# Optimization experiments

Measured on AMD Instinct MI355X. Metric: run time of the kernel, lower is better.

The kernel has to match this reference:

```python
import jax, jax.numpy as jnp
import numpy as np

B, S, D, H = 4, 2048, 2048, 16
DH = D // H


def setup_inputs() -> dict:
    key = jax.random.key(0)
    ks = jax.random.split(key, 11)
    p = 0.02  # keep pre-softmax logits in a sane range
    return {
        "x": jax.random.normal(ks[0], (B, S, D), jnp.float32),
        "Wq": jax.random.normal(ks[1], (D, D), jnp.float32) * p,
        "bq": jax.random.normal(ks[2], (D,), jnp.float32) * p,
        "Wk": jax.random.normal(ks[3], (D, D), jnp.float32) * p,
        "bk": jax.random.normal(ks[4], (D,), jnp.float32) * p,
        "Wv": jax.random.normal(ks[5], (D, D), jnp.float32) * p,
        "bv": jax.random.normal(ks[6], (D,), jnp.float32) * p,
        "Wo": jax.random.normal(ks[7], (D, D), jnp.float32) * p,
        "bo": jax.random.normal(ks[8], (D,), jnp.float32) * p,
        "spiral_weight": jax.random.normal(ks[9], (H,), jnp.float32),
        "helix_rotation": jax.random.normal(ks[10], (D,), jnp.float32),
    }


def reference(x, Wq, bq, Wk, bk, Wv, bv, Wo, bo, spiral_weight, helix_rotation):
    b, s, d = x.shape
    h, dh = H, d // H
    # projections (torch Linear: x @ W.T + b), split into heads
    q = (x @ Wq.T + bq).reshape(b, s, h, dh)
    k = (x @ Wk.T + bk).reshape(b, s, h, dh)
    v = (x @ Wv.T + bv).reshape(b, s, h, dh)
    # cos/sin helix gating, applied per (head, head_dim) channel
    rot = helix_rotation.reshape(h, dh)
    q = q * jnp.cos(rot)
    k = k * jnp.sin(rot)
    # per-head scaled scores: [b,h,s,s]
    scores = jnp.einsum("bshd,bthd->bhst", q, k) / np.sqrt(dh).astype(np.float32)
    scores = scores * spiral_weight[None, :, None, None]
    attn = jax.nn.softmax(scores, axis=-1)
    out = jnp.einsum("bhst,bthd->bshd", attn, v).reshape(b, s, d)
    return out @ Wo.T + bo
```

## Files before the change

kernel.cpp:

```cpp
#include <hip/hip_runtime.h>
#include <math.h>

#define B_ 4
#define S_ 2048
#define D_ 2048
#define H_ 16
#define DH_ 128

typedef unsigned short u16;
typedef unsigned int u32;
typedef u16 u16x8 __attribute__((ext_vector_type(8)));
typedef __bf16 bf16x8 __attribute__((ext_vector_type(8)));
typedef float f32x4 __attribute__((ext_vector_type(4)));

__device__ inline u16 f2bf(float f) {
    unsigned int u = __builtin_bit_cast(unsigned int, f);
    unsigned int lsb = (u >> 16) & 1u;
    u += 0x7fffu + lsb;
    return (u16)(u >> 16);
}

__device__ inline f32x4 mfma16(u16x8 a, u16x8 b, f32x4 c) {
    return __builtin_amdgcn_mfma_f32_16x16x32_bf16(
        __builtin_bit_cast(bf16x8, a), __builtin_bit_cast(bf16x8, b), c, 0, 0, 0);
}

__device__ inline void gl2lds16(const u16* g, u16* l) {
    __builtin_amdgcn_global_load_lds(
        (const __attribute__((address_space(1))) void*)g,
        (__attribute__((address_space(3))) void*)l, 16, 0, 0);
}

__device__ inline void block_barrier() {
    asm volatile("" ::: "memory");
    __builtin_amdgcn_s_barrier();
    asm volatile("" ::: "memory");
}

__global__ __launch_bounds__(256) void cvt_f32_bf16(const float* __restrict__ src,
                                                    u16* __restrict__ dst, int n8) {
    int i = blockIdx.x * 256 + threadIdx.x;
    if (i >= n8) return;
    const float4* s = (const float4*)src + (size_t)i * 2;
    float4 a = s[0], b = s[1];
    u16x8 o;
    o[0] = f2bf(a.x); o[1] = f2bf(a.y); o[2] = f2bf(a.z); o[3] = f2bf(a.w);
    o[4] = f2bf(b.x); o[5] = f2bf(b.y); o[6] = f2bf(b.z); o[7] = f2bf(b.w);
    *((u16x8*)dst + i) = o;
}

template <int GATE, int VOUT, typename OutT>
__global__ __launch_bounds__(512, 2) void gemm256(const u16* __restrict__ A,
                                                  const u16* __restrict__ Bw,
                                                  const float* __restrict__ bias,
                                                  const float* __restrict__ helix,
                                                  OutT* __restrict__ C,
                                                  int M, int N, int K) {
    __shared__ __align__(16) u16 As[2][256 * 64];
    __shared__ __align__(16) u16 Bs[2][256 * 64];

    const int tid = threadIdx.x;
    const int lane = tid & 63, w = tid >> 6;
    const int lr = lane & 15, quad = lane >> 4;
    const int wm = w & 1, wn = w >> 1;
    const int tm = blockIdx.y, tn = blockIdx.x;
    const int NT = K >> 6;

    const u16* Asrc = A + (size_t)(tm * 256) * K;
    const u16* Bsrc = Bw + (size_t)(tn * 256) * K;

    u32 go[4][2];
    u32 lo[4][2];
#pragma unroll
    for (int q = 0; q < 2; ++q) {
        const int seg = w * 2 + q;
        const int i0 = seg * 8 + (lane >> 3);
        const int s0 = seg * 8;
        int row = (i0 & 63) | ((i0 >> 6) << 7);
        int rb = (s0 & 63) | ((s0 >> 6) << 7);
        go[0][q] = (u32)row * K + (((lane & 7) ^ (row & 7)) << 3);
        lo[0][q] = rb << 6;
        row += 64; rb += 64;
        go[3][q] = (u32)row * K + (((lane & 7) ^ (row & 7)) << 3);
        lo[3][q] = rb << 6;
        row = (i0 & 31) | ((i0 >> 5) << 6);
        rb = (s0 & 31) | ((s0 >> 5) << 6);
        go[1][q] = (u32)row * K + (((lane & 7) ^ (row & 7)) << 3);
        lo[1][q] = rb << 6;
        row += 32; rb += 32;
        go[2][q] = (u32)row * K + (((lane & 7) ^ (row & 7)) << 3);
        lo[2][q] = rb << 6;
    }

#define STAGE(u, tt)                                                          \
    do {                                                                      \
        const int kt_ = (((tt) < NT) ? (tt) : (NT - 1)) << 6;                 \
        const u16* gb_ = ((u) == 1 || (u) == 2) ? Bsrc : Asrc;                \
        u16* lb_ = ((u) == 1 || (u) == 2) ? Bs[(tt) & 1] : As[(tt) & 1];      \
        gl2lds16(gb_ + go[u][0] + kt_, lb_ + lo[u][0]);                       \
        gl2lds16(gb_ + go[u][1] + kt_, lb_ + lo[u][1]);                       \
    } while (0)

    const int koff0 = (quad * 8) ^ ((lr & 7) * 8);
    const int koff1 = (32 + quad * 8) ^ ((lr & 7) * 8);
    const int rA = wm * 128 + lr;
    const int rB = wn * 64 + lr;

    f32x4 zero = {0.f, 0.f, 0.f, 0.f};
    f32x4 acc[8][4];
#pragma unroll
    for (int im = 0; im < 8; ++im)
#pragma unroll
        for (int jn = 0; jn < 4; ++jn) acc[im][jn] = zero;

    u16x8 af[4][2], bf[4][2];

    STAGE(0, 0); STAGE(1, 0); STAGE(2, 0); STAGE(3, 0);
    STAGE(0, 1); STAGE(1, 1); STAGE(2, 1);
    asm volatile("s_waitcnt vmcnt(6)" ::: "memory");
    block_barrier();

    for (int t = 0; t < NT; ++t) {
        const u16* Ab = As[t & 1];
        const u16* Bb = Bs[t & 1];

#pragma unroll
        for (int im = 0; im < 4; ++im) {
            af[im][0] = *(const u16x8*)&Ab[(rA + im * 16) * 64 + koff0];
            af[im][1] = *(const u16x8*)&Ab[(rA + im * 16) * 64 + koff1];
        }
#pragma unroll
        for (int jn = 0; jn < 2; ++jn) {
            bf[jn][0] = *(const u16x8*)&Bb[(rB + jn * 16) * 64 + koff0];
            bf[jn][1] = *(const u16x8*)&Bb[(rB + jn * 16) * 64 + koff1];
        }
        STAGE(3, t + 1);
        block_barrier();
        asm volatile("s_waitcnt lgkmcnt(0)" ::: "memory");
        __builtin_amdgcn_s_setprio(1);
#pragma unroll
        for (int s = 0; s < 2; ++s)
#pragma unroll
            for (int im = 0; im < 4; ++im)
#pragma unroll
                for (int jn = 0; jn < 2; ++jn)
                    acc[im][jn] = mfma16(af[im][s], bf[jn][s], acc[im][jn]);
        __builtin_amdgcn_s_setprio(0);
        block_barrier();

#pragma unroll
        for (int jn = 2; jn < 4; ++jn) {
            bf[jn][0] = *(const u16x8*)&Bb[(rB + jn * 16) * 64 + koff0];
            bf[jn][1] = *(const u16x8*)&Bb[(rB + jn * 16) * 64 + koff1];
        }
        STAGE(0, t + 2);
        block_barrier();
        asm volatile("s_waitcnt lgkmcnt(0)" ::: "memory");
        __builtin_amdgcn_s_setprio(1);
#pragma unroll
        for (int s = 0; s < 2; ++s)
#pragma unroll
            for (int im = 0; im < 4; ++im)
#pragma unroll
                for (int jn = 2; jn < 4; ++jn)
                    acc[im][jn] = mfma16(af[im][s], bf[jn][s], acc[im][jn]);
        __builtin_amdgcn_s_setprio(0);
        block_barrier();

#pragma unroll
        for (int im = 0; im < 4; ++im) {
            af[im][0] = *(const u16x8*)&Ab[(rA + 64 + im * 16) * 64 + koff0];
            af[im][1] = *(const u16x8*)&Ab[(rA + 64 + im * 16) * 64 + koff1];
        }
        STAGE(1, t + 2);
        block_barrier();
        asm volatile("s_waitcnt lgkmcnt(0)" ::: "memory");
        __builtin_amdgcn_s_setprio(1);
#pragma unroll
        for (int s = 0; s < 2; ++s)
#pragma unroll
            for (int im = 0; im < 4; ++im)
#pragma unroll
                for (int jn = 0; jn < 2; ++jn)
                    acc[im + 4][jn] = mfma16(af[im][s], bf[jn][s], acc[im + 4][jn]);
        __builtin_amdgcn_s_setprio(0);
        block_barrier();

        STAGE(2, t + 2);
        asm volatile("s_waitcnt vmcnt(6)" ::: "memory");
        block_barrier();
        __builtin_amdgcn_s_setprio(1);
#pragma unroll
        for (int s = 0; s < 2; ++s)
#pragma unroll
            for (int im = 0; im < 4; ++im)
#pragma unroll
                for (int jn = 2; jn < 4; ++jn)
                    acc[im + 4][jn] = mfma16(af[im][s], bf[jn][s], acc[im + 4][jn]);
        __builtin_amdgcn_s_setprio(0);
        block_barrier();
    }
    asm volatile("s_waitcnt vmcnt(0)" ::: "memory");
#undef STAGE

    if constexpr (VOUT) {
#pragma unroll
        for (int im = 0; im < 8; ++im)
#pragma unroll
            for (int r = 0; r < 4; ++r) {
                int row = tm * 256 + wm * 128 + im * 16 + quad * 4 + r;
                float bs = bias[row];
#pragma unroll
                for (int jn = 0; jn < 4; ++jn) {
                    int col = tn * 256 + wn * 64 + jn * 16 + lr;
                    float val = acc[im][jn][r] + bs;
                    ((u16*)C)[(size_t)(col >> 11) * ((size_t)D_ * S_) +
                              (size_t)row * S_ + (col & (S_ - 1))] = f2bf(val);
                }
            }
    } else {
#pragma unroll
        for (int jn = 0; jn < 4; ++jn) {
            int col = tn * 256 + wn * 64 + jn * 16 + lr;
            float bs = bias[col];
            float g = 1.0f;
            if (GATE == 1) g = cosf(helix[col]);
            if (GATE == 2) g = sinf(helix[col]);
#pragma unroll
            for (int im = 0; im < 8; ++im)
#pragma unroll
                for (int r = 0; r < 4; ++r) {
                    int row = tm * 256 + wm * 128 + im * 16 + quad * 4 + r;
                    float val = (acc[im][jn][r] + bs) * g;
                    if constexpr (sizeof(OutT) == 2)
                        ((u16*)C)[(size_t)row * N + col] = f2bf(val);
                    else
                        ((float*)C)[(size_t)row * N + col] = val;
                }
        }
    }
}

__global__ __launch_bounds__(256, 2) void helix_attn(const u16* __restrict__ Q,
                                                     const u16* __restrict__ Kq,
                                                     const u16* __restrict__ Vt,
                                                     const float* __restrict__ spiral,
                                                     u16* __restrict__ O) {
    __shared__ __align__(16) u16 Ks[64 * 136];
    __shared__ __align__(16) u16 Vs[128 * 72];
    __shared__ __align__(16) u16 Ps[128 * 80];

    const int tid = threadIdx.x;
    const int lane = tid & 63, w = tid >> 6;
    const int lr = lane & 15, quad = lane >> 4;

    const int bx = blockIdx.x;
    const int qt = bx & 15;
    const int h = (bx >> 4) & 15;
    const int b = bx >> 8;

    const size_t headoff = (size_t)b * S_ * D_ + (size_t)h * DH_;
    const u16* qp = Q + headoff;
    const u16* kp = Kq + headoff;
    const u16* vtp = Vt + ((size_t)b * H_ + h) * (size_t)DH_ * S_;

    const float scale2 = spiral[h] * 0.08838834764831845f * 1.4426950408889634f;

    u16x8 qf[2][4];
#pragma unroll
    for (int mb = 0; mb < 2; ++mb)
#pragma unroll
        for (int c = 0; c < 4; ++c) {
            u16x8 raw = *(const u16x8*)(qp + (size_t)(qt * 128 + mb * 64 + w * 16 + lr) * D_ +
                                        c * 32 + quad * 8);
#pragma unroll
            for (int j = 0; j < 8; ++j) {
                float f = __builtin_bit_cast(float, (u32)raw[j] << 16) * scale2;
                qf[mb][c][j] = f2bf(f);
            }
        }

    f32x4 zero = {0.f, 0.f, 0.f, 0.f};
    f32x4 Oacc[2][8];
#pragma unroll
    for (int mb = 0; mb < 2; ++mb)
#pragma unroll
        for (int n = 0; n < 8; ++n) Oacc[mb][n] = zero;
    float rs[2][4] = {{0.f, 0.f, 0.f, 0.f}, {0.f, 0.f, 0.f, 0.f}};

    for (int tt = 0; tt < 32; ++tt) {
        const int t0 = tt * 64;
        __syncthreads();
#pragma unroll
        for (int p = 0; p < 4; ++p) {
            int lin = p * 256 + tid;
            int trow = lin >> 4;
            int ch = (lin & 15) * 8;
            *(u16x8*)&Ks[trow * 136 + ch] =
                *(const u16x8*)(kp + (size_t)(t0 + trow) * D_ + ch);
            int drow = lin >> 3;
            int tch = (lin & 7) * 8;
            *(u16x8*)&Vs[drow * 72 + tch] =
                *(const u16x8*)(vtp + (size_t)drow * S_ + t0 + tch);
        }
        __syncthreads();

        f32x4 Sacc[2][4] = {{zero, zero, zero, zero}, {zero, zero, zero, zero}};
#pragma unroll
        for (int c = 0; c < 4; ++c) {
#pragma unroll
            for (int j = 0; j < 4; ++j) {
                u16x8 kf = *(const u16x8*)&Ks[(j * 16 + lr) * 136 + c * 32 + quad * 8];
                Sacc[0][j] = mfma16(qf[0][c], kf, Sacc[0][j]);
                Sacc[1][j] = mfma16(qf[1][c], kf, Sacc[1][j]);
            }
        }

#pragma unroll
        for (int mb = 0; mb < 2; ++mb)
#pragma unroll
            for (int j = 0; j < 4; ++j)
#pragma unroll
                for (int r = 0; r < 4; ++r) {
                    float p = exp2f(Sacc[mb][j][r]);
                    u32 u = __builtin_bit_cast(u32, p);
                    rs[mb][r] += __builtin_bit_cast(float, u & 0xffff0000u);
                    Ps[(mb * 64 + w * 16 + quad * 4 + r) * 80 + j * 16 + lr] = (u16)(u >> 16);
                }

#pragma unroll
        for (int ks = 0; ks < 2; ++ks) {
            u16x8 pf0 = *(const u16x8*)&Ps[(w * 16 + lr) * 80 + ks * 32 + quad * 8];
            u16x8 pf1 = *(const u16x8*)&Ps[(64 + w * 16 + lr) * 80 + ks * 32 + quad * 8];
#pragma unroll
            for (int n = 0; n < 8; ++n) {
                u16x8 vf = *(const u16x8*)&Vs[(n * 16 + lr) * 72 + ks * 32 + quad * 8];
                Oacc[0][n] = mfma16(pf0, vf, Oacc[0][n]);
                Oacc[1][n] = mfma16(pf1, vf, Oacc[1][n]);
            }
        }
    }

#pragma unroll
    for (int mb = 0; mb < 2; ++mb)
#pragma unroll
        for (int r = 0; r < 4; ++r) {
            float s = rs[mb][r];
#pragma unroll
            for (int off = 1; off < 16; off <<= 1) s += __shfl_xor(s, off, 64);
            float inv = 1.0f / s;
            int row = qt * 128 + mb * 64 + w * 16 + quad * 4 + r;
            u16* op = O + headoff + (size_t)row * D_;
#pragma unroll
            for (int n = 0; n < 8; ++n) op[n * 16 + lr] = f2bf(Oacc[mb][n][r] * inv);
        }
}

extern "C" void kernel_launch(void* const* d_in, const int* in_sizes, int n_in,
                              void* d_out, int out_size, void* d_ws, size_t ws_size,
                              hipStream_t stream) {
    const float* x = (const float*)d_in[0];
    const float* Wq = (const float*)d_in[1];
    const float* bq = (const float*)d_in[2];
    const float* Wk = (const float*)d_in[3];
    const float* bk = (const float*)d_in[4];
    const float* Wv = (const float*)d_in[5];
    const float* bv = (const float*)d_in[6];
    const float* Wo = (const float*)d_in[7];
    const float* bo = (const float*)d_in[8];
    const float* spiral = (const float*)d_in[9];
    const float* helix = (const float*)d_in[10];
    float* out = (float*)d_out;

    char* ws = (char*)d_ws;
    u16* xbf = (u16*)(ws);
    u16* wqb = (u16*)(ws + 33554432);
    u16* wkb = (u16*)(ws + 33554432 + 8388608);
    u16* wvb = (u16*)(ws + 33554432 + 16777216);
    u16* wob = (u16*)(ws + 33554432 + 25165824);
    u16* qb = (u16*)(ws + 67108864);
    u16* kb = (u16*)(ws + 67108864 + 33554432);
    u16* vtb = (u16*)(ws + 67108864 + 67108864);
    u16* attnb = xbf;

    const int ND = D_ * D_;
    const int NX = B_ * S_ * D_;

    cvt_f32_bf16<<<NX / 8 / 256, 256, 0, stream>>>(x, xbf, NX / 8);
    cvt_f32_bf16<<<ND / 8 / 256, 256, 0, stream>>>(Wq, wqb, ND / 8);
    cvt_f32_bf16<<<ND / 8 / 256, 256, 0, stream>>>(Wk, wkb, ND / 8);
    cvt_f32_bf16<<<ND / 8 / 256, 256, 0, stream>>>(Wv, wvb, ND / 8);
    cvt_f32_bf16<<<ND / 8 / 256, 256, 0, stream>>>(Wo, wob, ND / 8);

    dim3 gq(D_ / 256, (B_ * S_) / 256);
    gemm256<1, 0, u16><<<gq, 512, 0, stream>>>(xbf, wqb, bq, helix, qb, B_ * S_, D_, D_);
    gemm256<2, 0, u16><<<gq, 512, 0, stream>>>(xbf, wkb, bk, helix, kb, B_ * S_, D_, D_);
    dim3 gv((B_ * S_) / 256, D_ / 256);
    gemm256<0, 1, u16><<<gv, 512, 0, stream>>>(wvb, xbf, bv, nullptr, vtb, D_, B_ * S_, D_);

    helix_attn<<<B_ * H_ * (S_ / 128), 256, 0, stream>>>(qb, kb, vtb, spiral, attnb);

    gemm256<0, 0, float><<<gq, 512, 0, stream>>>(attnb, wob, bo, nullptr, out, B_ * S_, D_, D_);
}
```

Before: 703.2 us.

## Prefetch K/V tiles into registers, swizzle P smem layout, split attention launch

The attention kernel now loads the next K/V tile from global memory into registers while the current tile is being computed, so global latency is hidden behind the MFMA work. The P tile in shared memory uses an XOR-swizzled chunk layout to cut LDS bank conflicts on the scattered writes and vector reads. The attention launch is also split into two 512-block launches with a block offset. The register prefetch raises register pressure, which could hurt occupancy under the 256x2 launch bounds, and the extra launch adds a little overhead.

Result: no change. 715.4 us (+1.7%).

```diff
diff --git a/kernel.cpp b/kernel.cpp
--- a/kernel.cpp
+++ b/kernel.cpp
@@ -245,7 +245,7 @@
                                                      const u16* __restrict__ Kq,
                                                      const u16* __restrict__ Vt,
                                                      const float* __restrict__ spiral,
-                                                     u16* __restrict__ O) {
+                                                     u16* __restrict__ O, int bx0) {
     __shared__ __align__(16) u16 Ks[64 * 136];
     __shared__ __align__(16) u16 Vs[128 * 72];
     __shared__ __align__(16) u16 Ps[128 * 80];
@@ -254,7 +254,7 @@
     const int lane = tid & 63, w = tid >> 6;
     const int lr = lane & 15, quad = lane >> 4;
 
-    const int bx = blockIdx.x;
+    const int bx = blockIdx.x + bx0;
     const int qt = bx & 15;
     const int h = (bx >> 4) & 15;
     const int b = bx >> 8;
@@ -288,22 +288,36 @@
         for (int n = 0; n < 8; ++n) Oacc[mb][n] = zero;
     float rs[2][4] = {{0.f, 0.f, 0.f, 0.f}, {0.f, 0.f, 0.f, 0.f}};
 
+    u16x8 kst[4], vst[4];
+    int ktrow[4], kch[4], vdrow[4], vtch[4];
+#pragma unroll
+    for (int p = 0; p < 4; ++p) {
+        int lin = p * 256 + tid;
+        ktrow[p] = lin >> 4; kch[p] = (lin & 15) * 8;
+        vdrow[p] = lin >> 3; vtch[p] = (lin & 7) * 8;
+    }
+    auto issue_kv = [&](int t0_) {
+#pragma unroll
+        for (int p = 0; p < 4; ++p) {
+            kst[p] = *(const u16x8*)(kp + (size_t)(t0_ + ktrow[p]) * D_ + kch[p]);
+            vst[p] = *(const u16x8*)(vtp + (size_t)vdrow[p] * S_ + t0_ + vtch[p]);
+        }
+    };
+    issue_kv(0);
+
+    const int rsw = (lr >> 1) & 7;
+    const int wsw = (quad * 2) & 7;
+
     for (int tt = 0; tt < 32; ++tt) {
         const int t0 = tt * 64;
         __syncthreads();
 #pragma unroll
         for (int p = 0; p < 4; ++p) {
-            int lin = p * 256 + tid;
-            int trow = lin >> 4;
-            int ch = (lin & 15) * 8;
-            *(u16x8*)&Ks[trow * 136 + ch] =
-                *(const u16x8*)(kp + (size_t)(t0 + trow) * D_ + ch);
-            int drow = lin >> 3;
-            int tch = (lin & 7) * 8;
-            *(u16x8*)&Vs[drow * 72 + tch] =
-                *(const u16x8*)(vtp + (size_t)drow * S_ + t0 + tch);
+            *(u16x8*)&Ks[ktrow[p] * 136 + kch[p]] = kst[p];
+            *(u16x8*)&Vs[vdrow[p] * 72 + vtch[p]] = vst[p];
         }
         __syncthreads();
+        if (tt < 31) issue_kv(t0 + 64);
 
         f32x4 Sacc[2][4] = {{zero, zero, zero, zero}, {zero, zero, zero, zero}};
 #pragma unroll
@@ -325,13 +339,16 @@
                     float p = exp2f(Sacc[mb][j][r]);
                     u32 u = __builtin_bit_cast(u32, p);
                     rs[mb][r] += __builtin_bit_cast(float, u & 0xffff0000u);
-                    Ps[(mb * 64 + w * 16 + quad * 4 + r) * 80 + j * 16 + lr] = (u16)(u >> 16);
+                    int prow = mb * 64 + w * 16 + quad * 4 + r;
+                    int pchunk = (j * 2 + (lr >> 3)) ^ ((wsw + (r >> 1)) & 7);
+                    Ps[prow * 80 + pchunk * 8 + (lr & 7)] = (u16)(u >> 16);
                 }
 
 #pragma unroll
         for (int ks = 0; ks < 2; ++ks) {
-            u16x8 pf0 = *(const u16x8*)&Ps[(w * 16 + lr) * 80 + ks * 32 + quad * 8];
-            u16x8 pf1 = *(const u16x8*)&Ps[(64 + w * 16 + lr) * 80 + ks * 32 + quad * 8];
+            int pch = ((ks * 4 + quad) ^ rsw) * 8;
+            u16x8 pf0 = *(const u16x8*)&Ps[(w * 16 + lr) * 80 + pch];
+            u16x8 pf1 = *(const u16x8*)&Ps[(64 + w * 16 + lr) * 80 + pch];
 #pragma unroll
             for (int n = 0; n < 8; ++n) {
                 u16x8 vf = *(const u16x8*)&Vs[(n * 16 + lr) * 72 + ks * 32 + quad * 8];
@@ -398,7 +415,8 @@
     dim3 gv((B_ * S_) / 256, D_ / 256);
     gemm256<0, 1, u16><<<gv, 512, 0, stream>>>(wvb, xbf, bv, nullptr, vtb, D_, B_ * S_, D_);
 
-    helix_attn<<<B_ * H_ * (S_ / 128), 256, 0, stream>>>(qb, kb, vtb, spiral, attnb);
+    helix_attn<<<512, 256, 0, stream>>>(qb, kb, vtb, spiral, attnb, 0);
+    helix_attn<<<512, 256, 0, stream>>>(qb, kb, vtb, spiral, attnb, 512);
 
     gemm256<0, 0, float><<<gq, 512, 0, stream>>>(attnb, wob, bo, nullptr, out, B_ * S_, D_, D_);
 }
```
